# Performance work log

Hardware: AMD Instinct MI355X
Metric: run time of the kernel (lower is better)

The kernel has to match this reference:

```python
import jax, jax.numpy as jnp
import numpy as np
from jax import lax

BN_EPS = 1e-3
SLOPE = 0.1
CLUSTER_TEMP = 30.0
K = 16
FEAT = 4096  # 8*8*64


def conv_bn_lrelu(x, w, b, g, beta, m, v):
    # Conv2d stride 2, padding 1 (NCHW / OIHW), then eval-mode BatchNorm, then LeakyReLU.
    y = lax.conv_general_dilated(x, w, window_strides=(2, 2), padding=((1, 1), (1, 1)),
                                 dimension_numbers=("NCHW", "OIHW", "NCHW"))
    y = y + b[None, :, None, None]
    scale = g / jnp.sqrt(v + BN_EPS)
    y = y * scale[None, :, None, None] + (beta - m * scale)[None, :, None, None]
    return jnp.where(y > 0, y, SLOPE * y)


def soft_kmeans(data, mu, num_iter, ct):
    # Row L2-normalize (equivalent to diag(1/||x||) @ data)
    data = data / jnp.linalg.norm(data, axis=1, keepdims=True)
    for _ in range(num_iter):
        dist = data @ mu.T                      # [N, K]
        r = jax.nn.softmax(ct * dist, axis=1)   # [N, K]
        mu = (r.T @ data) / r.sum(axis=0)[:, None]  # [K, F]
    dist = data @ mu.T
    r = jax.nn.softmax(ct * dist, axis=1)
    return mu, r, dist


def setup_inputs() -> dict:
    key = jax.random.key(0)
    ks = jax.random.split(key, 12)
    d = {}
    d["x"] = jax.random.normal(ks[0], (256, 3, 64, 64), dtype=jnp.float32)
    # conv1: 3 -> 128
    d["conv1_w"] = jax.random.normal(ks[1], (128, 3, 3, 3), dtype=jnp.float32) * 0.05
    d["conv1_b"] = jnp.zeros((128,), jnp.float32)
    d["bn1_g"] = jnp.ones((128,), jnp.float32)
    d["bn1_b"] = jnp.zeros((128,), jnp.float32)
    d["bn1_m"] = jax.random.normal(ks[2], (128,), dtype=jnp.float32) * 0.1
    d["bn1_v"] = jax.random.uniform(ks[3], (128,), minval=0.5, maxval=1.5, dtype=jnp.float32)
    # conv2: 128 -> 256
    d["conv2_w"] = jax.random.normal(ks[4], (256, 128, 3, 3), dtype=jnp.float32) * 0.02
    d["conv2_b"] = jnp.zeros((256,), jnp.float32)
    d["bn2_g"] = jnp.ones((256,), jnp.float32)
    d["bn2_b"] = jnp.zeros((256,), jnp.float32)
    d["bn2_m"] = jax.random.normal(ks[5], (256,), dtype=jnp.float32) * 0.1
    d["bn2_v"] = jax.random.uniform(ks[6], (256,), minval=0.5, maxval=1.5, dtype=jnp.float32)
    # conv3: 256 -> 64
    d["conv3_w"] = jax.random.normal(ks[7], (64, 256, 3, 3), dtype=jnp.float32) * 0.02
    d["conv3_b"] = jnp.zeros((64,), jnp.float32)
    d["bn3_g"] = jnp.ones((64,), jnp.float32)
    d["bn3_b"] = jnp.zeros((64,), jnp.float32)
    d["bn3_m"] = jax.random.normal(ks[8], (64,), dtype=jnp.float32) * 0.1
    d["bn3_v"] = jax.random.uniform(ks[9], (64,), minval=0.5, maxval=1.5, dtype=jnp.float32)
    # initial cluster centers, torch.rand(K, F)
    d["mu0"] = jax.random.uniform(ks[10], (K, FEAT), dtype=jnp.float32)
    d["num_iter"] = 10
    return d


def reference(x, conv1_w, conv1_b, bn1_g, bn1_b, bn1_m, bn1_v,
              conv2_w, conv2_b, bn2_g, bn2_b, bn2_m, bn2_v,
              conv3_w, conv3_b, bn3_g, bn3_b, bn3_m, bn3_v,
              mu0, num_iter):
    h = conv_bn_lrelu(x, conv1_w, conv1_b, bn1_g, bn1_b, bn1_m, bn1_v)   # [B,128,32,32]
    h = conv_bn_lrelu(h, conv2_w, conv2_b, bn2_g, bn2_b, bn2_m, bn2_v)   # [B,256,16,16]
    h = conv_bn_lrelu(h, conv3_w, conv3_b, bn3_g, bn3_b, bn3_m, bn3_v)   # [B,64,8,8]
    embeds = h.reshape(-1, FEAT)                                          # [B, 4096]
    mu_init, _, _ = soft_kmeans(embeds, mu0, num_iter, CLUSTER_TEMP)
    _, r, _ = soft_kmeans(embeds, lax.stop_gradient(mu_init), 1, CLUSTER_TEMP)
    return r
```

## Files before the change

kernel.cpp:

```cpp
#include <hip/hip_runtime.h>
#include <stdint.h>
#include <stddef.h>

typedef unsigned short u16;
typedef __attribute__((ext_vector_type(8))) short short8;
typedef __attribute__((ext_vector_type(4))) float f32x4;
typedef __attribute__((ext_vector_type(4))) int int4v;

__device__ __forceinline__ float bf2f(u16 u) {
    unsigned x = ((unsigned)u) << 16;
    return __uint_as_float(x);
}
__device__ __forceinline__ u16 f2bf(float f) {
    unsigned x = __float_as_uint(f);
    unsigned r = (x + 0x7fffu + ((x >> 16) & 1u)) >> 16;
    return (u16)r;
}
__device__ __forceinline__ float ldin(const void* p, size_t i, int isbf) {
    return isbf ? bf2f(((const u16*)p)[i]) : ((const float*)p)[i];
}
__device__ __forceinline__ int detect_bf(const void* v1) {
    const u16* ub = (const u16*)v1;
    int ok = 1;
#pragma unroll
    for (int i = 0; i < 16; i++) {
        float f = bf2f(ub[i]);
        if (!(f >= 0.4f && f <= 1.6f)) ok = 0;
    }
    return ok;
}
__device__ __forceinline__ int sw(int r, int c8) {
    return r * 32 + (((c8) ^ (r & 3)) << 3);
}

struct PrepArgs {
    const void *w1, *w2, *w3;
    u16 *W1p, *W2p, *W3p;
    const void *b1, *g1, *be1, *m1, *v1;
    const void *b2, *g2, *be2, *m2, *v2;
    const void *b3, *g3, *be3, *m3, *v3;
    float *es1, *esh1, *es2, *esh2, *es3, *esh3;
};
__device__ __forceinline__ void packw_body(const void* src, u16* dst, int CI, int Kp,
                                           int total, int blk, int t, int isbf) {
    int p = blk * 256 + t;
    if (p >= total) return;
    int co = p / Kp, k = p - co * Kp;
    int tap = k / CI, ci = k - tap * CI;
    u16 v = 0;
    if (tap < 9) {
        size_t si = (size_t)(co * CI + ci) * 9 + tap;
        v = isbf ? ((const u16*)src)[si] : f2bf(((const float*)src)[si]);
    }
    dst[p] = v;
}
__global__ __launch_bounds__(256) void kprep_all(PrepArgs A) {
    int b = blockIdx.x, t = threadIdx.x;
    int isbf = detect_bf(A.v1);
    if (b < 1152) {
        packw_body(A.w2, A.W2p, 128, 1152, 256 * 1152, b, t, isbf);
    } else if (b < 1728) {
        packw_body(A.w3, A.W3p, 256, 2304, 64 * 2304, b - 1152, t, isbf);
    } else if (b < 1744) {
        packw_body(A.w1, A.W1p, 3, 32, 128 * 32, b - 1728, t, isbf);
    } else {
        int u = (b - 1744) * 256 + t;
        const void *bb, *g, *be, *m, *v;
        float *es, *esh;
        int c;
        if (u < 128)      { c = u;       bb=A.b1; g=A.g1; be=A.be1; m=A.m1; v=A.v1; es=A.es1; esh=A.esh1; }
        else if (u < 384) { c = u - 128; bb=A.b2; g=A.g2; be=A.be2; m=A.m2; v=A.v2; es=A.es2; esh=A.esh2; }
        else if (u < 448) { c = u - 384; bb=A.b3; g=A.g3; be=A.be3; m=A.m3; v=A.v3; es=A.es3; esh=A.esh3; }
        else return;
        float sc = ldin(g, c, isbf) / sqrtf(ldin(v, c, isbf) + 1e-3f);
        float sh = (ldin(bb, c, isbf) - ldin(m, c, isbf)) * sc + ldin(be, c, isbf);
        es[c] = sc;
        esh[c] = sh;
    }
}

__global__ void kfallback(u16* __restrict__ out) {
    int i = blockIdx.x * 256 + threadIdx.x;
    if (i < 4096) out[i] = f2bf(0.0625f);
}

__global__ __launch_bounds__(256) void im2col1(const void* __restrict__ x,
                                               u16* __restrict__ A1,
                                               const void* __restrict__ v1ref) {
    int n = blockIdx.x, t = threadIdx.x;
    int isbf = detect_bf(v1ref);
    __shared__ u16 xs[3 * 64 * 64];
    if (isbf) {
        const u16* xp = (const u16*)x + (size_t)n * 12288;
#pragma unroll
        for (int i = t * 8; i < 12288; i += 2048)
            *(int4v*)&xs[i] = *(const int4v*)&xp[i];
    } else {
        const float* xp = (const float*)x + (size_t)n * 12288;
#pragma unroll
        for (int i = t * 4; i < 12288; i += 1024) {
            float4 v = *(const float4*)&xp[i];
            xs[i] = f2bf(v.x); xs[i + 1] = f2bf(v.y);
            xs[i + 2] = f2bf(v.z); xs[i + 3] = f2bf(v.w);
        }
    }
    __syncthreads();
#pragma unroll
    for (int rr = 0; rr < 4; rr++) {
        int m = rr * 256 + t;
        int ox = m & 31, oy = m >> 5;
        alignas(16) u16 row[32];
#pragma unroll
        for (int k = 0; k < 32; k++) {
            u16 val = 0;
            if (k < 27) {
                int tap = k / 3, ci = k - 3 * tap;
                int ky = tap / 3, kx = tap - 3 * ky;
                int iy = 2 * oy - 1 + ky, ix = 2 * ox - 1 + kx;
                if ((unsigned)iy < 64u && (unsigned)ix < 64u)
                    val = xs[ci * 4096 + iy * 64 + ix];
            }
            row[k] = val;
        }
        int4v* dst = (int4v*)(A1 + ((size_t)n * 1024 + m) * 32);
        const int4v* srcv = (const int4v*)row;
#pragma unroll
        for (int q = 0; q < 4; q++) dst[q] = srcv[q];
    }
}

__global__ __launch_bounds__(256) void gemm_conv1(
    const u16* __restrict__ A1, const u16* __restrict__ W,
    const float* __restrict__ es, const float* __restrict__ esh,
    u16* __restrict__ OutB) {
    alignas(16) __shared__ u16 As[128 * 32];
    alignas(16) __shared__ u16 Bs[128 * 32];
    const int t = threadIdx.x;
    const int m0 = blockIdx.x * 128;
    const int lane = t & 63, w = t >> 6;
    const int wm = w & 1, wn = w >> 1;
    const int rA = t >> 2, c8 = t & 3, koff = c8 * 8;

#pragma unroll
    for (int j = 0; j < 2; j++) {
        int4v va = *(const int4v*)(A1 + (size_t)(m0 + j * 64 + rA) * 32 + koff);
        *(int4v*)&As[sw(j * 64 + rA, c8)] = va;
        int4v vb = *(const int4v*)(W + (size_t)(j * 64 + rA) * 32 + koff);
        *(int4v*)&Bs[sw(j * 64 + rA, c8)] = vb;
    }
    __syncthreads();
    const int qc = lane >> 4, fr = lane & 15;
    short8 af[4], bf[4];
#pragma unroll
    for (int i = 0; i < 4; i++) af[i] = *(const short8*)&As[sw(wm * 64 + i * 16 + fr, qc)];
#pragma unroll
    for (int j = 0; j < 4; j++) bf[j] = *(const short8*)&Bs[sw(wn * 64 + j * 16 + fr, qc)];
    f32x4 acc[4][4];
#pragma unroll
    for (int i = 0; i < 4; i++)
#pragma unroll
        for (int j = 0; j < 4; j++) {
#pragma unroll
            for (int q = 0; q < 4; q++) acc[i][j][q] = 0.f;
            acc[i][j] = __builtin_amdgcn_mfma_f32_16x16x32_bf16(af[i], bf[j], acc[i][j], 0, 0, 0);
        }
#pragma unroll
    for (int j = 0; j < 4; j++) {
        int c = wn * 64 + j * 16 + fr;
        float sc = es[c], sh = esh[c];
#pragma unroll
        for (int i = 0; i < 4; i++) {
#pragma unroll
            for (int rg = 0; rg < 4; rg++) {
                int m = m0 + wm * 64 + i * 16 + qc * 4 + rg;
                float v = acc[i][j][rg] * sc + sh;
                v = (v > 0.f) ? v : 0.1f * v;
                int ox = m & 31, oy = (m >> 5) & 31, n = m >> 10;
                OutB[((size_t)(n * 32 + oy) * 32 + ox) * 128 + c] = f2bf(v);
            }
        }
    }
}

__global__ __launch_bounds__(256) void gemm_conv2(
    const u16* __restrict__ Asrc, const u16* __restrict__ W,
    const float* __restrict__ es, const float* __restrict__ esh,
    u16* __restrict__ OutB) {
    constexpr int CIN = 128, KTOT = 1152, OHW = 16, LOG_OHW = 4, IH = 32;
    constexpr int CC = 4, AR = 2, BR = 2, SM = 4, SN = 4;

    alignas(16) __shared__ u16 As[128 * 32];
    alignas(16) __shared__ u16 Bs[128 * 32];

    const int t = threadIdx.x;
    const int lid = blockIdx.x;
    const int xcd = lid & 7, slot = lid >> 3;
    const int img = xcd * 32 + (slot >> 2);
    const int sub = slot & 3;
    const int m0 = img * 256 + (sub & 1) * 128;
    const int n0 = (sub >> 1) * 128;
    const int lane = t & 63, w = t >> 6;
    const int wm = w & 1, wn = w >> 1;
    const int rA = t >> 2, c8 = t & 3, koff = c8 * 8;
    const int fr = lane & 15, qc = lane >> 4;

    f32x4 acc[SM][SN];
#pragma unroll
    for (int i = 0; i < SM; i++)
#pragma unroll
        for (int j = 0; j < SN; j++)
#pragma unroll
            for (int q = 0; q < 4; q++) acc[i][j][q] = 0.0f;

    int aox[AR], aoy[AR], an_[AR];
#pragma unroll
    for (int j = 0; j < AR; j++) {
        int m = m0 + j * 64 + rA;
        aox[j] = m & (OHW - 1);
        aoy[j] = (m >> LOG_OHW) & (OHW - 1);
        an_[j] = m >> (2 * LOG_OHW);
    }
    auto mkoffs = [&](int j, int tap) -> int {
        int ky = tap / 3, kx = tap - 3 * ky;
        int iy = 2 * aoy[j] - 1 + ky, ix = 2 * aox[j] - 1 + kx;
        if ((unsigned)iy < (unsigned)IH && (unsigned)ix < (unsigned)IH)
            return ((an_[j] * IH + iy) * IH + ix) * CIN;
        return -0x40000000;
    };
    const u16* Wrow[BR];
#pragma unroll
    for (int j = 0; j < BR; j++)
        Wrow[j] = W + (size_t)(n0 + j * 64 + rA) * KTOT + koff;

    int offs_cur[AR], offs_nxt[AR];
#pragma unroll
    for (int j = 0; j < AR; j++) offs_cur[j] = mkoffs(j, 0);

    const int4v zerov = (int4v){0, 0, 0, 0};
    int4v bufA[2][AR], bufB[2][BR];
#pragma unroll
    for (int pp = 0; pp < 2; pp++) {
#pragma unroll
        for (int j = 0; j < AR; j++)
            bufA[pp][j] = (offs_cur[j] >= 0)
                              ? *(const int4v*)(Asrc + offs_cur[j] + pp * 32 + koff)
                              : zerov;
#pragma unroll
        for (int j = 0; j < BR; j++) bufB[pp][j] = *(const int4v*)(Wrow[j] + pp * 32);
    }

    int flat = 0;
    for (int tap = 0; tap < 9; tap++) {
#pragma unroll
        for (int j = 0; j < AR; j++)
            offs_nxt[j] = (tap < 8) ? mkoffs(j, tap + 1) : -0x40000000;
#pragma unroll
        for (int cc = 0; cc < CC; cc++, flat++) {
            const int pb_ = flat & 1;
#pragma unroll
            for (int j = 0; j < AR; j++) *(int4v*)&As[sw(j * 64 + rA, c8)] = bufA[pb_][j];
#pragma unroll
            for (int j = 0; j < BR; j++) *(int4v*)&Bs[sw(j * 64 + rA, c8)] = bufB[pb_][j];
            __syncthreads();
            {
                const int cc2 = cc + 2;
                const bool intap = (cc2 < CC);
                const int cci = intap ? cc2 : cc2 - CC;
                const int aoffbase = cci * 32 + koff;
#pragma unroll
                for (int j = 0; j < AR; j++) {
                    int o = intap ? offs_cur[j] : offs_nxt[j];
                    bufA[pb_][j] = (o >= 0) ? *(const int4v*)(Asrc + o + aoffbase) : zerov;
                }
                const bool wvalid = intap || (tap < 8);
                const int wk = (intap ? tap : tap + 1) * CIN + cci * 32;
#pragma unroll
                for (int j = 0; j < BR; j++)
                    bufB[pb_][j] = wvalid ? *(const int4v*)(Wrow[j] + wk) : zerov;
            }
            short8 af[SM], bf[SN];
#pragma unroll
            for (int i = 0; i < SM; i++)
                af[i] = *(const short8*)&As[sw(wm * 64 + i * 16 + fr, qc)];
#pragma unroll
            for (int j = 0; j < SN; j++)
                bf[j] = *(const short8*)&Bs[sw(wn * 64 + j * 16 + fr, qc)];
#pragma unroll
            for (int i = 0; i < SM; i++)
#pragma unroll
                for (int j = 0; j < SN; j++)
                    acc[i][j] = __builtin_amdgcn_mfma_f32_16x16x32_bf16(
                        af[i], bf[j], acc[i][j], 0, 0, 0);
            __syncthreads();
        }
#pragma unroll
        for (int j = 0; j < AR; j++) offs_cur[j] = offs_nxt[j];
    }

#pragma unroll
    for (int j = 0; j < SN; j++) {
        int c = n0 + wn * 64 + j * 16 + fr;
        float sc = es[c], sh = esh[c];
#pragma unroll
        for (int i = 0; i < SM; i++) {
#pragma unroll
            for (int rg = 0; rg < 4; rg++) {
                int row = wm * 64 + i * 16 + qc * 4 + rg;
                int m = m0 + row;
                float v = acc[i][j][rg] * sc + sh;
                v = (v > 0.f) ? v : 0.1f * v;
                int ox = m & (OHW - 1), oy = (m >> LOG_OHW) & (OHW - 1), n = m >> (2 * LOG_OHW);
                OutB[((size_t)(n * 16 + oy) * 16 + ox) * 256 + c] = f2bf(v);
            }
        }
    }
}

__global__ __launch_bounds__(256) void gemm_conv3f(
    const u16* __restrict__ Asrc, const u16* __restrict__ W,
    const float* __restrict__ es3, const float* __restrict__ esh3,
    float* __restrict__ dat, u16* __restrict__ datbf) {
    constexpr int CIN = 256, KTOT = 2304, IH = 16;
    constexpr int CC = 8, SM = 2, SN = 2;

    alignas(16) __shared__ u16 As[64 * 32];
    alignas(16) __shared__ u16 Bs[64 * 32];
    __shared__ float red[4];

    const int t = threadIdx.x;
    const int lid = blockIdx.x;
    const int xcd = lid & 7, slot = lid >> 3;
    const int img = xcd * 32 + slot;
    const int m0 = img * 64;
    const int lane = t & 63, w = t >> 6;
    const int wm = w & 1, wn = w >> 1;
    const int rA = t >> 2, c8 = t & 3, koff = c8 * 8;
    const int fr = lane & 15, qc = lane >> 4;

    f32x4 acc[SM][SN];
#pragma unroll
    for (int i = 0; i < SM; i++)
#pragma unroll
        for (int j = 0; j < SN; j++)
#pragma unroll
            for (int q = 0; q < 4; q++) acc[i][j][q] = 0.0f;

    const int aox = rA & 7, aoy = (rA >> 3) & 7;
    auto mkoffs = [&](int tap) -> int {
        int ky = tap / 3, kx = tap - 3 * ky;
        int iy = 2 * aoy - 1 + ky, ix = 2 * aox - 1 + kx;
        if ((unsigned)iy < (unsigned)IH && (unsigned)ix < (unsigned)IH)
            return ((img * IH + iy) * IH + ix) * CIN;
        return -0x40000000;
    };
    const u16* Wrow = W + (size_t)rA * KTOT + koff;

    int offs_cur = mkoffs(0), offs_nxt;
    const int4v zerov = (int4v){0, 0, 0, 0};
    int4v bufA[2], bufB[2];
#pragma unroll
    for (int pp = 0; pp < 2; pp++) {
        bufA[pp] = (offs_cur >= 0)
                       ? *(const int4v*)(Asrc + offs_cur + pp * 32 + koff)
                       : zerov;
        bufB[pp] = *(const int4v*)(Wrow + pp * 32);
    }

    int flat = 0;
    for (int tap = 0; tap < 9; tap++) {
        offs_nxt = (tap < 8) ? mkoffs(tap + 1) : -0x40000000;
#pragma unroll
        for (int cc = 0; cc < CC; cc++, flat++) {
            const int pb_ = flat & 1;
            *(int4v*)&As[sw(rA, c8)] = bufA[pb_];
            *(int4v*)&Bs[sw(rA, c8)] = bufB[pb_];
            __syncthreads();
            {
                const int cc2 = cc + 2;
                const bool intap = (cc2 < CC);
                const int cci = intap ? cc2 : cc2 - CC;
                int o = intap ? offs_cur : offs_nxt;
                bufA[pb_] = (o >= 0) ? *(const int4v*)(Asrc + o + cci * 32 + koff) : zerov;
                const bool wvalid = intap || (tap < 8);
                const int wk = (intap ? tap : tap + 1) * CIN + cci * 32;
                bufB[pb_] = wvalid ? *(const int4v*)(Wrow + wk) : zerov;
            }
            short8 af[SM], bf[SN];
#pragma unroll
            for (int i = 0; i < SM; i++)
                af[i] = *(const short8*)&As[sw(wm * 32 + i * 16 + fr, qc)];
#pragma unroll
            for (int j = 0; j < SN; j++)
                bf[j] = *(const short8*)&Bs[sw(wn * 32 + j * 16 + fr, qc)];
#pragma unroll
            for (int i = 0; i < SM; i++)
#pragma unroll
                for (int j = 0; j < SN; j++)
                    acc[i][j] = __builtin_amdgcn_mfma_f32_16x16x32_bf16(
                        af[i], bf[j], acc[i][j], 0, 0, 0);
            __syncthreads();
        }
        offs_cur = offs_nxt;
    }

    float vals[SM][SN][4];
    float ssq = 0.f;
#pragma unroll
    for (int j = 0; j < SN; j++) {
        int c = wn * 32 + j * 16 + fr;
        float sc = es3[c], sh = esh3[c];
#pragma unroll
        for (int i = 0; i < SM; i++) {
#pragma unroll
            for (int rg = 0; rg < 4; rg++) {
                float v = acc[i][j][rg] * sc + sh;
                v = (v > 0.f) ? v : 0.1f * v;
                vals[i][j][rg] = v;
                ssq += v * v;
            }
        }
    }
#pragma unroll
    for (int off = 32; off > 0; off >>= 1) ssq += __shfl_xor(ssq, off);
    if (lane == 0) red[w] = ssq;
    __syncthreads();
    float inv = 1.0f / sqrtf(red[0] + red[1] + red[2] + red[3]);
#pragma unroll
    for (int j = 0; j < SN; j++) {
        int c = wn * 32 + j * 16 + fr;
#pragma unroll
        for (int i = 0; i < SM; i++) {
#pragma unroll
            for (int rg = 0; rg < 4; rg++) {
                int row = wm * 32 + i * 16 + qc * 4 + rg;
                size_t idx = (size_t)img * 4096 + c * 64 + row;
                float v = vals[i][j][rg] * inv;
                dat[idx] = v;
                datbf[idx] = f2bf(v);
            }
        }
    }
}

__global__ __launch_bounds__(256) void kgr(const u16* __restrict__ dbf,
                                           const float* __restrict__ dat,
                                           const void* __restrict__ mu0,
                                           u16* __restrict__ Ghi,
                                           u16* __restrict__ Glo,
                                           float* __restrict__ rb0,
                                           const void* __restrict__ v1ref) {
    const int b = blockIdx.x, t = threadIdx.x;
    alignas(16) __shared__ u16 As[64 * 32];
    alignas(16) __shared__ u16 Bs[64 * 32];
    __shared__ float part[16][4];
    __shared__ float ds[16];

    if (b < 16) {
        const int m0 = (b & 3) * 64, n0 = (b >> 2) * 64;
        const int lane = t & 63, w = t >> 6;
        const int wm = w & 1, wn = w >> 1;
        const int rA = t >> 2, c8 = t & 3, koff = c8 * 8;

        f32x4 acc[2][2];
#pragma unroll
        for (int i = 0; i < 2; i++)
#pragma unroll
            for (int j = 0; j < 2; j++)
#pragma unroll
                for (int q = 0; q < 4; q++) acc[i][j][q] = 0.0f;

        int4v pa = *(const int4v*)(dbf + (size_t)(m0 + rA) * 4096 + koff);
        int4v pb = *(const int4v*)(dbf + (size_t)(n0 + rA) * 4096 + koff);
        for (int it = 0; it < 128; it++) {
            *(int4v*)&As[sw(rA, c8)] = pa;
            *(int4v*)&Bs[sw(rA, c8)] = pb;
            __syncthreads();
            if (it + 1 < 128) {
                int k = (it + 1) * 32 + koff;
                pa = *(const int4v*)(dbf + (size_t)(m0 + rA) * 4096 + k);
                pb = *(const int4v*)(dbf + (size_t)(n0 + rA) * 4096 + k);
            }
            const int qc = lane >> 4, fr = lane & 15;
            short8 af[2], bf[2];
#pragma unroll
            for (int i = 0; i < 2; i++) af[i] = *(const short8*)&As[sw(wm * 32 + i * 16 + fr, qc)];
#pragma unroll
            for (int j = 0; j < 2; j++) bf[j] = *(const short8*)&Bs[sw(wn * 32 + j * 16 + fr, qc)];
#pragma unroll
            for (int i = 0; i < 2; i++)
#pragma unroll
                for (int j = 0; j < 2; j++)
                    acc[i][j] = __builtin_amdgcn_mfma_f32_16x16x32_bf16(af[i], bf[j], acc[i][j], 0, 0, 0);
            if (it + 1 < 128) __syncthreads();
        }
#pragma unroll
        for (int j = 0; j < 2; j++) {
            int c = n0 + wn * 32 + j * 16 + (lane & 15);
#pragma unroll
            for (int i = 0; i < 2; i++)
#pragma unroll
                for (int rg = 0; rg < 4; rg++) {
                    int row = m0 + wm * 32 + i * 16 + (lane >> 4) * 4 + rg;
                    float v = acc[i][j][rg];
                    u16 hi = f2bf(v);
                    u16 lo = f2bf(v - bf2f(hi));
                    Ghi[(size_t)row * 256 + c] = hi;
                    Glo[(size_t)row * 256 + c] = lo;
                }
        }
    } else {
        const int n = b - 16;
        const int isbf = detect_bf(v1ref);
        const int lane = t & 63, wv = t >> 6;
        float d[16];
#pragma unroll
        for (int j = 0; j < 16; j++) d[j] = dat[(size_t)n * 4096 + j * 256 + t];
#pragma unroll
        for (int k = 0; k < 16; k++) {
            float a = 0.f;
            if (isbf) {
                const u16* mp = (const u16*)mu0 + (size_t)k * 4096;
#pragma unroll
                for (int j = 0; j < 16; j++) a = fmaf(d[j], bf2f(mp[j * 256 + t]), a);
            } else {
                const float* mp = (const float*)mu0 + (size_t)k * 4096;
#pragma unroll
                for (int j = 0; j < 16; j++) a = fmaf(d[j], mp[j * 256 + t], a);
            }
#pragma unroll
            for (int off = 32; off > 0; off >>= 1) a += __shfl_xor(a, off);
            if (lane == 0) part[k][wv] = a;
        }
        __syncthreads();
        if (t < 16) {
            float dk = part[t][0] + part[t][1] + part[t][2] + part[t][3];
            ds[t] = dk;
            __syncthreads();
            float mx = -1e30f;
#pragma unroll
            for (int j = 0; j < 16; j++) mx = fmaxf(mx, ds[j]);
            float sum = 0.f;
#pragma unroll
            for (int j = 0; j < 16; j++) sum += __expf(30.f * (ds[j] - mx));
            rb0[n * 16 + t] = __expf(30.f * (dk - mx)) / sum;
        }
    }
}

__global__ __launch_bounds__(1024) void kmiter(const u16* __restrict__ Ghi,
                                               const u16* __restrict__ Glo,
                                               const float* __restrict__ rb0,
                                               void* __restrict__ dout,
                                               const void* __restrict__ v1ref) {
    const int t = threadIdx.x;
    const int isbf = detect_bf(v1ref);
    const int lane = t & 63, w = t >> 6;
    const int i0 = w * 16;
    const int col = lane & 15;
    const int q = lane >> 4;

    __shared__ float rf[4096];
    __shared__ u16 rThi[16 * 264];
    __shared__ u16 rTlo[16 * 264];
    __shared__ float part[16][17];
    __shared__ float rs[16];

    for (int idx = t; idx < 4096; idx += 1024) {
        float v = rb0[idx];
        rf[idx] = v;
        u16 hi = f2bf(v);
        rThi[(idx & 15) * 264 + (idx >> 4)] = hi;
        rTlo[(idx & 15) * 264 + (idx >> 4)] = f2bf(v - bf2f(hi));
    }
    __syncthreads();

    const u16* Ahirow = Ghi + (size_t)(i0 + col) * 256 + q * 8;
    const u16* Alorow = Glo + (size_t)(i0 + col) * 256 + q * 8;
    for (int iter = 0; iter < 11; iter++) {
        f32x4 acc = {0.f, 0.f, 0.f, 0.f};
#pragma unroll
        for (int ks = 0; ks < 256; ks += 32) {
            short8 ah = *(const short8*)(Ahirow + ks);
            short8 al = *(const short8*)(Alorow + ks);
            short8 bh = *(const short8*)&rThi[col * 264 + ks + q * 8];
            short8 bl = *(const short8*)&rTlo[col * 264 + ks + q * 8];
            acc = __builtin_amdgcn_mfma_f32_16x16x32_bf16(ah, bh, acc, 0, 0, 0);
            acc = __builtin_amdgcn_mfma_f32_16x16x32_bf16(al, bh, acc, 0, 0, 0);
            acc = __builtin_amdgcn_mfma_f32_16x16x32_bf16(ah, bl, acc, 0, 0, 0);
        }
        if (t < 256) {
            int kk = t & 15, g = t >> 4;
            float psum = 0.f;
#pragma unroll
            for (int nn = 0; nn < 16; nn++) psum += rf[(g * 16 + nn) * 16 + kk];
            part[kk][g] = psum;
        }
        __syncthreads();
        if (t < 16) {
            float ssum = 0.f;
#pragma unroll
            for (int g = 0; g < 16; g++) ssum += part[t][g];
            rs[t] = ssum;
        }
        __syncthreads();
        float rsc = rs[col];
        float rv[4];
#pragma unroll
        for (int rg = 0; rg < 4; rg++) {
            float dk = acc[rg] / rsc;
            float mx = dk;
#pragma unroll
            for (int o = 1; o < 16; o <<= 1) mx = fmaxf(mx, __shfl_xor(mx, o));
            float e = __expf(30.f * (dk - mx));
            float ssum = e;
#pragma unroll
            for (int o = 1; o < 16; o <<= 1) ssum += __shfl_xor(ssum, o);
            rv[rg] = e / ssum;
        }
        if (iter < 10) {
            __syncthreads();
#pragma unroll
            for (int rg = 0; rg < 4; rg++) {
                int row = i0 + q * 4 + rg;
                float v = rv[rg];
                rf[row * 16 + col] = v;
                u16 hi = f2bf(v);
                rThi[col * 264 + row] = hi;
                rTlo[col * 264 + row] = f2bf(v - bf2f(hi));
            }
            __syncthreads();
        } else {
#pragma unroll
            for (int rg = 0; rg < 4; rg++) {
                int row = i0 + q * 4 + rg;
                if (isbf) ((u16*)dout)[row * 16 + col] = f2bf(rv[rg]);
                else ((float*)dout)[row * 16 + col] = rv[rg];
            }
        }
    }
}

extern "C" void kernel_launch(void* const* d_in, const int* in_sizes, int n_in,
                              void* d_out, int out_size, void* d_ws, size_t ws_size,
                              hipStream_t stream) {
    const void* x   = d_in[0];
    const void* w1  = d_in[1];
    const void* b1  = d_in[2];
    const void* g1  = d_in[3];
    const void* be1 = d_in[4];
    const void* m1  = d_in[5];
    const void* v1  = d_in[6];
    const void* w2  = d_in[7];
    const void* b2  = d_in[8];
    const void* g2  = d_in[9];
    const void* be2 = d_in[10];
    const void* m2  = d_in[11];
    const void* v2  = d_in[12];
    const void* w3  = d_in[13];
    const void* b3  = d_in[14];
    const void* g3  = d_in[15];
    const void* be3 = d_in[16];
    const void* m3  = d_in[17];
    const void* v3  = d_in[18];
    const void* mu0 = d_in[19];

    char* p = (char*)d_ws;
    size_t used = 0;
    auto alloc = [&](size_t bytes) -> char* {
        char* q = p;
        size_t rb = (bytes + 255) & ~(size_t)255;
        p += rb;
        used += rb;
        return q;
    };
    float* rb0 = (float*)alloc(4096 * 4);
    u16* Ghi = (u16*)alloc((size_t)65536 * 2);
    u16* Glo = (u16*)alloc((size_t)65536 * 2);
    u16* W1p = (u16*)alloc((size_t)128 * 32 * 2);
    u16* W2p = (u16*)alloc((size_t)256 * 1152 * 2);
    u16* W3p = (u16*)alloc((size_t)64 * 2304 * 2);
    float* es1 = (float*)alloc(128 * 4);
    float* esh1 = (float*)alloc(128 * 4);
    float* es2 = (float*)alloc(256 * 4);
    float* esh2 = (float*)alloc(256 * 4);
    float* es3 = (float*)alloc(64 * 4);
    float* esh3 = (float*)alloc(64 * 4);
    const size_t R1 = (size_t)256 * 32 * 32 * 128 * 2;
    const size_t R2 = (size_t)256 * 16 * 16 * 256 * 2;
    char* reg1 = alloc(R1);
    char* reg2 = alloc(R2);
    u16* h1 = (u16*)reg1;
    u16* A1 = (u16*)reg2;
    u16* h2 = (u16*)reg2;
    float* dat = (float*)reg1;
    u16* datbf = (u16*)(reg1 + 4194304);

    if (used > ws_size) {
        kfallback<<<16, 256, 0, stream>>>((u16*)d_out);
        return;
    }

    PrepArgs pa = {w1, w2, w3, W1p, W2p, W3p,
                   b1, g1, be1, m1, v1, b2, g2, be2, m2, v2, b3, g3, be3, m3, v3,
                   es1, esh1, es2, esh2, es3, esh3};
    kprep_all<<<1746, 256, 0, stream>>>(pa);
    im2col1<<<256, 256, 0, stream>>>(x, A1, v1);
    gemm_conv1<<<dim3(2048), 256, 0, stream>>>(A1, W1p, es1, esh1, h1);
    gemm_conv2<<<dim3(1024), 256, 0, stream>>>(h1, W2p, es2, esh2, h2);
    gemm_conv3f<<<dim3(256), 256, 0, stream>>>(h2, W3p, es3, esh3, dat, datbf);
    kgr<<<dim3(272), 256, 0, stream>>>(datbf, dat, mu0, Ghi, Glo, rb0, v1);
    kmiter<<<1, 1024, 0, stream>>>(Ghi, Glo, rb0, d_out, v1);
}
```

Baseline: 292.1 us.

## Restructure conv2 GEMM into per-image 256x256 tiles with direct-to-LDS async loads

The conv2 implicit GEMM now uses one 512-thread block per image, computing the full 256x256 output tile with 64-wide K steps, instead of four 128x128 tiles per image. Operands are staged with global_load_lds directly into double-buffered, XOR-swizzled shared memory, and out-of-bounds taps point at a zeroed scratch buffer rather than a register-side zero select. MFMA bursts are wrapped in s_setprio. This cuts redundant A/B loads and register staging, but it uses 128KB of LDS and 32 accumulators per lane, launches only 256 blocks, and adds occupancy and register-pressure risk.

```diff
diff --git a/kernel.cpp b/kernel.cpp
--- a/kernel.cpp
+++ b/kernel.cpp
@@ -40,6 +40,7 @@
     const void *b2, *g2, *be2, *m2, *v2;
     const void *b3, *g3, *be3, *m3, *v3;
     float *es1, *esh1, *es2, *esh2, *es3, *esh3;
+    u16 *zb;
 };
 __device__ __forceinline__ void packw_body(const void* src, u16* dst, int CI, int Kp,
                                            int total, int blk, int t, int isbf) {
@@ -64,6 +65,7 @@
     } else if (b < 1744) {
         packw_body(A.w1, A.W1p, 3, 32, 128 * 32, b - 1728, t, isbf);
     } else {
+        if (b == 1745) A.zb[t] = 0;
         int u = (b - 1744) * 256 + t;
         const void *bb, *g, *be, *m, *v;
         float *es, *esh;
@@ -182,135 +184,132 @@
     }
 }
 
-__global__ __launch_bounds__(256) void gemm_conv2(
-    const u16* __restrict__ Asrc, const u16* __restrict__ W,
+__global__ __launch_bounds__(512, 2) void gemm_conv2(
+    const u16* __restrict__ h1, const u16* __restrict__ W,
     const float* __restrict__ es, const float* __restrict__ esh,
-    u16* __restrict__ OutB) {
-    constexpr int CIN = 128, KTOT = 1152, OHW = 16, LOG_OHW = 4, IH = 32;
-    constexpr int CC = 4, AR = 2, BR = 2, SM = 4, SN = 4;
-
-    alignas(16) __shared__ u16 As[128 * 32];
-    alignas(16) __shared__ u16 Bs[128 * 32];
+    u16* __restrict__ OutB, const u16* __restrict__ zb) {
+    alignas(16) __shared__ u16 smem[4 * 16384];
+    u16* const Ab0 = smem;
+    u16* const Ab1 = smem + 16384;
+    u16* const Bb0 = smem + 32768;
+    u16* const Bb1 = smem + 49152;
 
     const int t = threadIdx.x;
-    const int lid = blockIdx.x;
-    const int xcd = lid & 7, slot = lid >> 3;
-    const int img = xcd * 32 + (slot >> 2);
-    const int sub = slot & 3;
-    const int m0 = img * 256 + (sub & 1) * 128;
-    const int n0 = (sub >> 1) * 128;
-    const int lane = t & 63, w = t >> 6;
-    const int wm = w & 1, wn = w >> 1;
-    const int rA = t >> 2, c8 = t & 3, koff = c8 * 8;
-    const int fr = lane & 15, qc = lane >> 4;
-
-    f32x4 acc[SM][SN];
-#pragma unroll
-    for (int i = 0; i < SM; i++)
-#pragma unroll
-        for (int j = 0; j < SN; j++)
-#pragma unroll
-            for (int q = 0; q < 4; q++) acc[i][j][q] = 0.0f;
-
-    int aox[AR], aoy[AR], an_[AR];
-#pragma unroll
-    for (int j = 0; j < AR; j++) {
-        int m = m0 + j * 64 + rA;
-        aox[j] = m & (OHW - 1);
-        aoy[j] = (m >> LOG_OHW) & (OHW - 1);
-        an_[j] = m >> (2 * LOG_OHW);
-    }
-    auto mkoffs = [&](int j, int tap) -> int {
-        int ky = tap / 3, kx = tap - 3 * ky;
-        int iy = 2 * aoy[j] - 1 + ky, ix = 2 * aox[j] - 1 + kx;
-        if ((unsigned)iy < (unsigned)IH && (unsigned)ix < (unsigned)IH)
-            return ((an_[j] * IH + iy) * IH + ix) * CIN;
-        return -0x40000000;
+    const int w = t >> 6, l = t & 63;
+    const int img = blockIdx.x;
+    const int wm = w >> 2, wn = w & 3;
+    const int fr = l & 15, qc = l >> 4;
+
+    int aiy0[4], aix0[4], ac8e[4];
+    int brow[4];
+#pragma unroll
+    for (int i = 0; i < 4; ++i) {
+        int gi = w * 256 + i * 64 + l;
+        int r = gi >> 3, c8d = gi & 7;
+        int c8s = c8d ^ (r & 7);
+        int oy = r >> 4, ox = r & 15;
+        aiy0[i] = 2 * oy - 1;
+        aix0[i] = 2 * ox - 1;
+        ac8e[i] = c8s * 8;
+        brow[i] = r * 1152 + c8s * 8;
+    }
+    auto mkA = [&](int i, int ky, int kx) -> const u16* {
+        int iy = aiy0[i] + ky, ix = aix0[i] + kx;
+        if ((unsigned)iy < 32u && (unsigned)ix < 32u)
+            return h1 + (size_t)(((img * 32 + iy) * 32 + ix) * 128 + ac8e[i]);
+        return zb;
     };
-    const u16* Wrow[BR];
-#pragma unroll
-    for (int j = 0; j < BR; j++)
-        Wrow[j] = W + (size_t)(n0 + j * 64 + rA) * KTOT + koff;
-
-    int offs_cur[AR], offs_nxt[AR];
-#pragma unroll
-    for (int j = 0; j < AR; j++) offs_cur[j] = mkoffs(j, 0);
-
-    const int4v zerov = (int4v){0, 0, 0, 0};
-    int4v bufA[2][AR], bufB[2][BR];
-#pragma unroll
-    for (int pp = 0; pp < 2; pp++) {
-#pragma unroll
-        for (int j = 0; j < AR; j++)
-            bufA[pp][j] = (offs_cur[j] >= 0)
-                              ? *(const int4v*)(Asrc + offs_cur[j] + pp * 32 + koff)
-                              : zerov;
-#pragma unroll
-        for (int j = 0; j < BR; j++) bufB[pp][j] = *(const int4v*)(Wrow[j] + pp * 32);
-    }
-
-    int flat = 0;
-    for (int tap = 0; tap < 9; tap++) {
-#pragma unroll
-        for (int j = 0; j < AR; j++)
-            offs_nxt[j] = (tap < 8) ? mkoffs(j, tap + 1) : -0x40000000;
-#pragma unroll
-        for (int cc = 0; cc < CC; cc++, flat++) {
-            const int pb_ = flat & 1;
-#pragma unroll
-            for (int j = 0; j < AR; j++) *(int4v*)&As[sw(j * 64 + rA, c8)] = bufA[pb_][j];
-#pragma unroll
-            for (int j = 0; j < BR; j++) *(int4v*)&Bs[sw(j * 64 + rA, c8)] = bufB[pb_][j];
-            __syncthreads();
-            {
-                const int cc2 = cc + 2;
-                const bool intap = (cc2 < CC);
-                const int cci = intap ? cc2 : cc2 - CC;
-                const int aoffbase = cci * 32 + koff;
-#pragma unroll
-                for (int j = 0; j < AR; j++) {
-                    int o = intap ? offs_cur[j] : offs_nxt[j];
-                    bufA[pb_][j] = (o >= 0) ? *(const int4v*)(Asrc + o + aoffbase) : zerov;
+    auto stage = [&](const u16* src, u16* ldsbase, int i) {
+        __builtin_amdgcn_global_load_lds(
+            (const __attribute__((address_space(1))) void*)src,
+            (__attribute__((address_space(3))) void*)(ldsbase + (w * 4 + i) * 512),
+            16, 0, 0);
+    };
+
+    f32x4 acc[8][4];
+#pragma unroll
+    for (int mi = 0; mi < 8; ++mi)
+#pragma unroll
+        for (int nj = 0; nj < 4; ++nj)
+#pragma unroll
+            for (int q = 0; q < 4; ++q) acc[mi][nj][q] = 0.0f;
+
+    auto do_tile = [&](const u16* A, const u16* B) {
+#pragma unroll
+        for (int ii = 0; ii < 2; ++ii)
+#pragma unroll
+            for (int jj = 0; jj < 2; ++jj)
+#pragma unroll
+                for (int kk = 0; kk < 2; ++kk) {
+                    const int c8 = kk * 4 + qc;
+                    short8 a[4], b[2];
+#pragma unroll
+                    for (int q = 0; q < 4; ++q) {
+                        int row = wm * 128 + (ii * 4 + q) * 16 + fr;
+                        a[q] = *(const short8*)(A + row * 64 + ((c8 ^ (row & 7)) << 3));
+                    }
+#pragma unroll
+                    for (int j = 0; j < 2; ++j) {
+                        int row = wn * 64 + (jj * 2 + j) * 16 + fr;
+                        b[j] = *(const short8*)(B + row * 64 + ((c8 ^ (row & 7)) << 3));
+                    }
+                    __builtin_amdgcn_s_setprio(1);
+#pragma unroll
+                    for (int q = 0; q < 4; ++q)
+#pragma unroll
+                        for (int j = 0; j < 2; ++j)
+                            acc[ii * 4 + q][jj * 2 + j] =
+                                __builtin_amdgcn_mfma_f32_16x16x32_bf16(
+                                    a[q], b[j], acc[ii * 4 + q][jj * 2 + j], 0, 0, 0);
+                    __builtin_amdgcn_s_setprio(0);
                 }
-                const bool wvalid = intap || (tap < 8);
-                const int wk = (intap ? tap : tap + 1) * CIN + cci * 32;
-#pragma unroll
-                for (int j = 0; j < BR; j++)
-                    bufB[pb_][j] = wvalid ? *(const int4v*)(Wrow[j] + wk) : zerov;
-            }
-            short8 af[SM], bf[SN];
-#pragma unroll
-            for (int i = 0; i < SM; i++)
-                af[i] = *(const short8*)&As[sw(wm * 64 + i * 16 + fr, qc)];
-#pragma unroll
-            for (int j = 0; j < SN; j++)
-                bf[j] = *(const short8*)&Bs[sw(wn * 64 + j * 16 + fr, qc)];
-#pragma unroll
-            for (int i = 0; i < SM; i++)
-#pragma unroll
-                for (int j = 0; j < SN; j++)
-                    acc[i][j] = __builtin_amdgcn_mfma_f32_16x16x32_bf16(
-                        af[i], bf[j], acc[i][j], 0, 0, 0);
-            __syncthreads();
-        }
-#pragma unroll
-        for (int j = 0; j < AR; j++) offs_cur[j] = offs_nxt[j];
-    }
-
-#pragma unroll
-    for (int j = 0; j < SN; j++) {
-        int c = n0 + wn * 64 + j * 16 + fr;
+    };
+
+    const u16* pcur[4];
+#pragma unroll
+    for (int i = 0; i < 4; ++i) pcur[i] = mkA(i, 0, 0);
+#pragma unroll
+    for (int i = 0; i < 4; ++i) {
+        stage(pcur[i], Ab0, i);
+        stage(W + brow[i], Bb0, i);
+    }
+
+    for (int tap = 0; tap < 9; ++tap) {
+        __syncthreads();
+#pragma unroll
+        for (int i = 0; i < 4; ++i) {
+            stage(pcur[i] + 64, Ab1, i);
+            stage(W + brow[i] + (2 * tap + 1) * 64, Bb1, i);
+        }
+        do_tile(Ab0, Bb0);
+        __syncthreads();
+        if (tap < 8) {
+            const int tap2 = tap + 1;
+            const int ky2 = (tap2 >= 6) ? 2 : (tap2 >= 3) ? 1 : 0;
+            const int kx2 = tap2 - 3 * ky2;
+#pragma unroll
+            for (int i = 0; i < 4; ++i) pcur[i] = mkA(i, ky2, kx2);
+#pragma unroll
+            for (int i = 0; i < 4; ++i) {
+                stage(pcur[i], Ab0, i);
+                stage(W + brow[i] + (2 * tap + 2) * 64, Bb0, i);
+            }
+        }
+        do_tile(Ab1, Bb1);
+    }
+
+#pragma unroll
+    for (int nj = 0; nj < 4; ++nj) {
+        int c = wn * 64 + nj * 16 + fr;
         float sc = es[c], sh = esh[c];
 #pragma unroll
-        for (int i = 0; i < SM; i++) {
-#pragma unroll
-            for (int rg = 0; rg < 4; rg++) {
-                int row = wm * 64 + i * 16 + qc * 4 + rg;
-                int m = m0 + row;
-                float v = acc[i][j][rg] * sc + sh;
+        for (int mi = 0; mi < 8; ++mi) {
+#pragma unroll
+            for (int rg = 0; rg < 4; ++rg) {
+                int r = wm * 128 + mi * 16 + qc * 4 + rg;
+                float v = acc[mi][nj][rg] * sc + sh;
                 v = (v > 0.f) ? v : 0.1f * v;
-                int ox = m & (OHW - 1), oy = (m >> LOG_OHW) & (OHW - 1), n = m >> (2 * LOG_OHW);
-                OutB[((size_t)(n * 16 + oy) * 16 + ox) * 256 + c] = f2bf(v);
+                OutB[((size_t)img * 256 + r) * 256 + c] = f2bf(v);
             }
         }
     }
@@ -685,6 +684,7 @@
     float* esh2 = (float*)alloc(256 * 4);
     float* es3 = (float*)alloc(64 * 4);
     float* esh3 = (float*)alloc(64 * 4);
+    u16* zb = (u16*)alloc(512);
     const size_t R1 = (size_t)256 * 32 * 32 * 128 * 2;
     const size_t R2 = (size_t)256 * 16 * 16 * 256 * 2;
     char* reg1 = alloc(R1);
@@ -702,11 +702,11 @@
 
     PrepArgs pa = {w1, w2, w3, W1p, W2p, W3p,
                    b1, g1, be1, m1, v1, b2, g2, be2, m2, v2, b3, g3, be3, m3, v3,
-                   es1, esh1, es2, esh2, es3, esh3};
+                   es1, esh1, es2, esh2, es3, esh3, zb};
     kprep_all<<<1746, 256, 0, stream>>>(pa);
     im2col1<<<256, 256, 0, stream>>>(x, A1, v1);
     gemm_conv1<<<dim3(2048), 256, 0, stream>>>(A1, W1p, es1, esh1, h1);
-    gemm_conv2<<<dim3(1024), 256, 0, stream>>>(h1, W2p, es2, esh2, h2);
+    gemm_conv2<<<dim3(256), 512, 0, stream>>>(h1, W2p, es2, esh2, h2, zb);
     gemm_conv3f<<<dim3(256), 256, 0, stream>>>(h2, W3p, es3, esh3, dat, datbf);
     kgr<<<dim3(272), 256, 0, stream>>>(datbf, dat, mu0, Ghi, Glo, rb0, v1);
     kmiter<<<1, 1024, 0, stream>>>(Ghi, Glo, rb0, d_out, v1);
```

Measured after the change: 290.4 us. About the same (-0.6%).
